# Optimization experiments

Hardware: AMD Instinct MI355X
Metric: run time of the kernel (lower is better)

## Reference

```python
import jax, jax.numpy as jnp
import numpy as np

B, S, D, H = 8, 1024, 1024, 16
DH = D // H  # 64
SCALE = (DH // H) ** (-0.5)  # faithful to torch: (key.size(-1) // num_heads) ** -0.5 = 4**-0.5 = 0.5
LN_EPS = 1e-5


def setup_inputs() -> dict:
    key = jax.random.key(0)
    ks = jax.random.split(key, 12)
    f = jnp.float32
    return {
        "key":   jax.random.normal(ks[0], (B, S, D), f),
        "value": jax.random.normal(ks[1], (B, S, D), f),
        "query": jax.random.normal(ks[2], (B, S, D), f),
        "Wq": jax.random.normal(ks[3], (D, D), f) * 0.02,
        "bq": jnp.zeros((D,), f),
        "Wk": jax.random.normal(ks[4], (D, D), f) * 0.02,
        "bk": jnp.zeros((D,), f),
        "Wv": jax.random.normal(ks[5], (D, D), f) * 0.02,
        "bv": jnp.zeros((D,), f),
        "Wo": jax.random.normal(ks[6], (D, D), f) * 0.02,
        "bo": jnp.zeros((D,), f),
        "ln_gamma": jnp.ones((D,), f),
        "ln_beta": jnp.zeros((D,), f),
    }


def _layer_norm(x, gamma, beta):
    mu = jnp.mean(x, axis=-1, keepdims=True)
    var = jnp.mean(jnp.square(x - mu), axis=-1, keepdims=True)
    return (x - mu) * jax.lax.rsqrt(var + LN_EPS) * gamma + beta


def reference(key, value, query, Wq, bq, Wk, bk, Wv, bv, Wo, bo, ln_gamma, ln_beta):
    residual = query
    # QKV projections (torch Linear: x @ W.T + b)
    k = key @ Wk.T + bk
    v = value @ Wv.T + bv
    q = query @ Wq.T + bq
    # Faithful raw view [B,S,H*dh] -> [B*H, S, dh] (row-major reshape, as in torch .view)
    k = k.reshape(B * H, S, DH)
    v = v.reshape(B * H, S, DH)
    q = q.reshape(B * H, S, DH)
    # scores: [B*H, S, S], softmax over last axis (dim=2)
    attn = jnp.einsum("bid,bjd->bij", q, k) * SCALE
    attn = jax.nn.softmax(attn, axis=2)
    context = jnp.einsum("bij,bjd->bid", attn, v)
    context = context.reshape(B, S, D)  # faithful raw view back
    out = context @ Wo.T + bo
    out = _layer_norm(residual + out, ln_gamma, ln_beta)
    return out, attn
```

## Files before the change

### kernel.cpp

```cpp
#include <hip/hip_runtime.h>
#include <stdint.h>

typedef unsigned short ushort_t;
typedef __attribute__((ext_vector_type(8))) short s16x8;
typedef __attribute__((ext_vector_type(8))) unsigned short u16x8;
typedef __attribute__((ext_vector_type(4))) unsigned short u16x4;
typedef __attribute__((ext_vector_type(4))) float f32x4;

#define AS1C(p) ((const __attribute__((address_space(1))) void*)(p))
#define AS3(p)  ((__attribute__((address_space(3))) void*)(p))

#define QSCALE 0.7213475204444817f

#define EXP2F(x) __builtin_amdgcn_exp2f(x)
#define LOG2F(x) __builtin_amdgcn_logf(x)

#define WAVE_LDS_FENCE()                                    \
  do {                                                      \
    asm volatile("s_waitcnt lgkmcnt(0)" ::: "memory");      \
    __builtin_amdgcn_sched_barrier(0);                      \
  } while (0)

#define SBAR()                                              \
  do {                                                      \
    __builtin_amdgcn_sched_barrier(0);                      \
    __builtin_amdgcn_s_barrier();                           \
    __builtin_amdgcn_sched_barrier(0);                      \
  } while (0)

__device__ __forceinline__ ushort_t f2bf(float f) {
  uint32_t u = __float_as_uint(f);
  u += 0x7fffu + ((u >> 16) & 1u);
  return (ushort_t)(u >> 16);
}
__device__ __forceinline__ float bf2f(ushort_t h) {
  return __uint_as_float(((uint32_t)h) << 16);
}

__global__ __launch_bounds__(256) void cvt3_kernel(const float* __restrict__ s0,
                                                   const float* __restrict__ s1,
                                                   const float* __restrict__ s2,
                                                   ushort_t* __restrict__ dst) {
  const int y = blockIdx.y;
  const float* src = y == 0 ? s0 : (y == 1 ? s1 : s2);
  const int i = blockIdx.x * 256 + threadIdx.x;
  const float4 v = ((const float4*)src)[i];
  ushort4 o;
  o.x = f2bf(v.x); o.y = f2bf(v.y); o.z = f2bf(v.z); o.w = f2bf(v.w);
  ((ushort4*)(dst + (size_t)y * 8388608))[i] = o;
}

__global__ __launch_bounds__(256) void cvtw_kernel(const float* __restrict__ w0,
                                                   const float* __restrict__ w1,
                                                   const float* __restrict__ w2,
                                                   const float* __restrict__ w3,
                                                   ushort_t* __restrict__ dqkv,
                                                   ushort_t* __restrict__ dwo) {
  const int y = blockIdx.y;
  const float* src = y == 0 ? w0 : (y == 1 ? w1 : (y == 2 ? w2 : w3));
  ushort_t* dst = y < 3 ? dqkv + (size_t)y * 1048576 : dwo;
  const float sc = y == 0 ? QSCALE : 1.0f;
  const int i = blockIdx.x * 256 + threadIdx.x;
  const float4 v = ((const float4*)src)[i];
  ushort4 o;
  o.x = f2bf(v.x * sc); o.y = f2bf(v.y * sc); o.z = f2bf(v.z * sc); o.w = f2bf(v.w * sc);
  ((ushort4*)dst)[i] = o;
}

__global__ __launch_bounds__(256) void biascat_kernel(const float* __restrict__ bq,
                                                      const float* __restrict__ bk,
                                                      const float* __restrict__ bv,
                                                      float* __restrict__ dst) {
  const int i = blockIdx.x * 256 + threadIdx.x;
  dst[i] = i < 1024 ? bq[i] * QSCALE : (i < 2048 ? bk[i - 1024] : bv[i - 2048]);
}

template <int OUT_BF16>
__global__ __launch_bounds__(512) void gemm_nt(const ushort_t* __restrict__ A0,
                                               const ushort_t* __restrict__ A1,
                                               const ushort_t* __restrict__ A2,
                                               const ushort_t* __restrict__ B,
                                               const float* __restrict__ bias,
                                               void* __restrict__ C0,
                                               void* __restrict__ C1,
                                               void* __restrict__ C2) {
  __shared__ ushort_t As[3][128 * 32];
  __shared__ ushort_t Bs[3][128 * 32];
  const int tid = threadIdx.x;
  const int w = tid >> 6, lane = tid & 63, g = lane >> 4, c = lane & 15;
  const int wm = w >> 1, wn = w & 1;
  const int m0 = blockIdx.y * 128, n0 = blockIdx.x * 128;
  const int sel = n0 >> 10, nloc0 = n0 & 1023;
  const ushort_t* A = sel == 0 ? A0 : (sel == 1 ? A1 : A2);
  char* C = (char*)(sel == 0 ? C0 : (sel == 1 ? C1 : C2));
  f32x4 acc[2][4] = {};

  const int srow = tid >> 2, scol = (tid & 3) << 3;
  const int sdst = (w * 64) * 8;

#define G_STAGE(buf, k0_)                                                                  \
  do {                                                                                     \
    __builtin_amdgcn_global_load_lds(AS1C(&A[(size_t)(m0 + srow) * 1024 + (k0_) + scol]),  \
                                     AS3(&As[buf][sdst]), 16, 0, 0);                       \
    __builtin_amdgcn_global_load_lds(AS1C(&B[(size_t)(n0 + srow) * 1024 + (k0_) + scol]),  \
                                     AS3(&Bs[buf][sdst]), 16, 0, 0);                       \
  } while (0)

  G_STAGE(0, 0);
  G_STAGE(1, 32);
  asm volatile("s_waitcnt vmcnt(2)" ::: "memory");
  SBAR();
  int cur = 0;
  for (int it = 0; it < 32; ++it) {
    if (it < 30) {
      const int sb = cur >= 1 ? cur - 1 : 2;
      G_STAGE(sb, 32 * (it + 2));
    }
    s16x8 af[2], bfr[4];
#pragma unroll
    for (int mi = 0; mi < 2; ++mi)
      af[mi] = *(const s16x8*)&As[cur][(wm * 32 + mi * 16 + c) * 32 + g * 8];
#pragma unroll
    for (int ni = 0; ni < 4; ++ni)
      bfr[ni] = *(const s16x8*)&Bs[cur][(wn * 64 + ni * 16 + c) * 32 + g * 8];
    __builtin_amdgcn_s_setprio(1);
#pragma unroll
    for (int mi = 0; mi < 2; ++mi)
#pragma unroll
      for (int ni = 0; ni < 4; ++ni)
        acc[mi][ni] = __builtin_amdgcn_mfma_f32_16x16x32_bf16(af[mi], bfr[ni], acc[mi][ni], 0, 0, 0);
    __builtin_amdgcn_s_setprio(0);
    if (it < 31) {
      if (it < 30)
        asm volatile("s_waitcnt vmcnt(2) lgkmcnt(0)" ::: "memory");
      else
        asm volatile("s_waitcnt vmcnt(0) lgkmcnt(0)" ::: "memory");
      SBAR();
    }
    cur = cur < 2 ? cur + 1 : 0;
  }
#undef G_STAGE

#pragma unroll
  for (int ni = 0; ni < 4; ++ni) {
    const int nn = wn * 64 + ni * 16 + c;
    const float bv = bias[n0 + nn];
#pragma unroll
    for (int mi = 0; mi < 2; ++mi) {
#pragma unroll
      for (int rr = 0; rr < 4; ++rr) {
        const int m = m0 + wm * 32 + mi * 16 + g * 4 + rr;
        const float val = acc[mi][ni][rr] + bv;
        if (OUT_BF16)
          ((ushort_t*)C)[(size_t)m * 1024 + nloc0 + nn] = f2bf(val);
        else
          ((float*)C)[(size_t)m * 1024 + nloc0 + nn] = val;
      }
    }
  }
}

__global__ __launch_bounds__(256) void transpose_v(const ushort_t* __restrict__ v,
                                                   ushort_t* __restrict__ vt) {
  __shared__ ushort_t T[64][72];
  const int n = blockIdx.y, ib = blockIdx.x;
  const int t = threadIdx.x;
  {
    const int row = t >> 2, cb = (t & 3) << 4;
    const ushort_t* src = v + (size_t)n * 65536 + (size_t)(ib * 64 + row) * 64 + cb;
    *(u16x8*)&T[row][cb] = *(const u16x8*)src;
    *(u16x8*)&T[row][cb + 8] = *(const u16x8*)(src + 8);
  }
  __syncthreads();
  {
    const int dh = t >> 2, ibs = (t & 3) << 4;
    u16x8 a, b;
#pragma unroll
    for (int e = 0; e < 8; ++e) { a[e] = T[ibs + e][dh]; b[e] = T[ibs + 8 + e][dh]; }
    ushort_t* dst = vt + (size_t)n * 65536 + (size_t)dh * 1024 + ib * 64 + ibs;
    *(u16x8*)dst = a;
    *(u16x8*)(dst + 8) = b;
  }
}

__global__ __launch_bounds__(256) void stats_kernel(const ushort_t* __restrict__ q,
                                                    const ushort_t* __restrict__ k,
                                                    float* __restrict__ bias_out) {
  __shared__ ushort_t Kb[3][64 * 64];
  const int wg = blockIdx.x;
  const int idx = ((wg & 7) << 6) | (wg >> 3);
  const int n = idx >> 2, qb = idx & 3;
  const int tid = threadIdx.x, w = tid >> 6, lane = tid & 63, g = lane >> 4, c = lane & 15;
  const int q0 = qb * 256 + w * 64;
  const ushort_t* qh = q + (size_t)n * 65536;
  const char* khb = (const char*)(k + (size_t)n * 65536);

  const int r0 = w * 16 + (lane >> 3);
  const int csw = (((lane & 7) ^ (lane >> 3)) << 4);

#define STAGE_KS(buf, jt_)                                                                  \
  do {                                                                                      \
    __builtin_amdgcn_global_load_lds(AS1C(khb + ((size_t)(jt_)*64 + r0) * 128 + csw),       \
                                     AS3(&Kb[buf][(w * 2 + 0) * 512]), 16, 0, 0);           \
    __builtin_amdgcn_global_load_lds(AS1C(khb + ((size_t)(jt_)*64 + r0 + 8) * 128 + csw),   \
                                     AS3(&Kb[buf][(w * 2 + 1) * 512]), 16, 0, 0);           \
  } while (0)
#define KFRAGS(buf, jn, h)                                                    \
  (*(const s16x8*)((const char*)&Kb[buf][0] +                                 \
                   (((((jn)*16 + c) * 128 + (h)*64 + g * 16)) ^ ((c & 7) << 4))))

  s16x8 aq[4][2];
#pragma unroll
  for (int fr = 0; fr < 4; ++fr) {
    aq[fr][0] = *(const s16x8*)&qh[(q0 + fr * 16 + c) * 64 + g * 8];
    aq[fr][1] = *(const s16x8*)&qh[(q0 + fr * 16 + c) * 64 + 32 + g * 8];
  }

  float l_acc[4][4] = {};

  STAGE_KS(0, 0);
  STAGE_KS(1, 1);
  asm volatile("s_waitcnt vmcnt(2)" ::: "memory");
  SBAR();
  int cur = 0;
  for (int jt = 0; jt < 16; ++jt) {
    if (jt < 14) {
      const int sb = cur >= 1 ? cur - 1 : 2;
      STAGE_KS(sb, jt + 2);
    }
#pragma unroll
    for (int fr = 0; fr < 4; ++fr) {
      f32x4 sfr[4];
      __builtin_amdgcn_s_setprio(1);
#pragma unroll
      for (int jn = 0; jn < 4; ++jn) {
        f32x4 z = {0.f, 0.f, 0.f, 0.f};
        z = __builtin_amdgcn_mfma_f32_16x16x32_bf16(aq[fr][0], KFRAGS(cur, jn, 0), z, 0, 0, 0);
        z = __builtin_amdgcn_mfma_f32_16x16x32_bf16(aq[fr][1], KFRAGS(cur, jn, 1), z, 0, 0, 0);
        sfr[jn] = z;
      }
      __builtin_amdgcn_s_setprio(0);
#pragma unroll
      for (int rr = 0; rr < 4; ++rr)
        l_acc[fr][rr] += EXP2F(sfr[0][rr]) + EXP2F(sfr[1][rr]) +
                         EXP2F(sfr[2][rr]) + EXP2F(sfr[3][rr]);
    }
    if (jt < 15) {
      if (jt < 14)
        asm volatile("s_waitcnt vmcnt(2) lgkmcnt(0)" ::: "memory");
      else
        asm volatile("s_waitcnt vmcnt(0) lgkmcnt(0)" ::: "memory");
      SBAR();
    }
    cur = cur < 2 ? cur + 1 : 0;
  }

#pragma unroll
  for (int fr = 0; fr < 4; ++fr)
#pragma unroll
    for (int rr = 0; rr < 4; ++rr) {
      float l = l_acc[fr][rr];
      l += __shfl_xor(l, 1);
      l += __shfl_xor(l, 2);
      l += __shfl_xor(l, 4);
      l += __shfl_xor(l, 8);
      if (c == 0)
        bias_out[(size_t)n * 1024 + q0 + fr * 16 + g * 4 + rr] = LOG2F(l);
    }
#undef STAGE_KS
#undef KFRAGS
}

__global__ __launch_bounds__(256) void attn_kernel(const ushort_t* __restrict__ q,
                                                   const ushort_t* __restrict__ k,
                                                   const ushort_t* __restrict__ vt,
                                                   const float* __restrict__ stats,
                                                   float* __restrict__ attn,
                                                   ushort_t* __restrict__ ctx) {
  __shared__ ushort_t Kb[2][64 * 64];
  __shared__ ushort_t Vb[2][64 * 64];
  __shared__ ushort_t Pb[4][16 * 64];
  const int wg = blockIdx.x;
  const int idx = ((wg & 7) << 7) | (wg >> 3);
  const int n = idx >> 3, qb = idx & 7;
  const int tid = threadIdx.x, w = tid >> 6, lane = tid & 63, g = lane >> 4, c = lane & 15;
  const int i0 = qb * 128 + w * 32;
  const ushort_t* qh = q + (size_t)n * 65536;
  const char* khb = (const char*)(k + (size_t)n * 65536);
  const char* vhb = (const char*)(vt + (size_t)n * 65536);
  char* pwb = (char*)&Pb[w][0];

  const int r0 = w * 16 + (lane >> 3);
  const int csw = (((lane & 7) ^ (lane >> 3)) << 4);

#define STAGE_K(buf, jt_)                                                                   \
  do {                                                                                      \
    __builtin_amdgcn_global_load_lds(AS1C(khb + ((size_t)(jt_)*64 + r0) * 128 + csw),       \
                                     AS3(&Kb[buf][(w * 2 + 0) * 512]), 16, 0, 0);           \
    __builtin_amdgcn_global_load_lds(AS1C(khb + ((size_t)(jt_)*64 + r0 + 8) * 128 + csw),   \
                                     AS3(&Kb[buf][(w * 2 + 1) * 512]), 16, 0, 0);           \
  } while (0)
#define STAGE_V(buf, jt_)                                                                   \
  do {                                                                                      \
    __builtin_amdgcn_global_load_lds(AS1C(vhb + (size_t)r0 * 2048 + (jt_)*128 + csw),       \
                                     AS3(&Vb[buf][(w * 2 + 0) * 512]), 16, 0, 0);           \
    __builtin_amdgcn_global_load_lds(AS1C(vhb + (size_t)(r0 + 8) * 2048 + (jt_)*128 + csw), \
                                     AS3(&Vb[buf][(w * 2 + 1) * 512]), 16, 0, 0);           \
  } while (0)
#define KFRAG(buf, jn, h)                                                     \
  (*(const s16x8*)((const char*)&Kb[buf][0] +                                 \
                   (((((jn)*16 + c) * 128 + (h)*64 + g * 16)) ^ ((c & 7) << 4))))
#define VFRAG(buf, dn, ks_)                                                   \
  (*(const s16x8*)((const char*)&Vb[buf][0] +                                 \
                   (((((dn)*16 + c) * 128 + (ks_)*64 + g * 16)) ^ ((c & 7) << 4))))

  s16x8 aq[2][2];
  float bias_r[2][4];
#pragma unroll
  for (int fr = 0; fr < 2; ++fr) {
    aq[fr][0] = *(const s16x8*)&qh[(i0 + fr * 16 + c) * 64 + g * 8];
    aq[fr][1] = *(const s16x8*)&qh[(i0 + fr * 16 + c) * 64 + 32 + g * 8];
    const float* sb = stats + (size_t)n * 1024 + i0 + fr * 16;
#pragma unroll
    for (int r = 0; r < 4; ++r) bias_r[fr][r] = sb[4 * g + r];
  }

  f32x4 cacc[2][4] = {};
  float* arow = attn + (size_t)n * 1048576;

  STAGE_K(0, 0);
  STAGE_V(0, 0);
  asm volatile("s_waitcnt vmcnt(0) lgkmcnt(0)" ::: "memory");
  SBAR();
  for (int jt = 0; jt < 16; ++jt) {
    const int cur = jt & 1;
    if (jt < 15) { STAGE_K(cur ^ 1, jt + 1); STAGE_V(cur ^ 1, jt + 1); }
    f32x4 s[2][4];
    __builtin_amdgcn_s_setprio(1);
#pragma unroll
    for (int fr = 0; fr < 2; ++fr)
#pragma unroll
      for (int jn = 0; jn < 4; ++jn) {
        f32x4 z = {0.f, 0.f, 0.f, 0.f};
        z = __builtin_amdgcn_mfma_f32_16x16x32_bf16(aq[fr][0], KFRAG(cur, jn, 0), z, 0, 0, 0);
        z = __builtin_amdgcn_mfma_f32_16x16x32_bf16(aq[fr][1], KFRAG(cur, jn, 1), z, 0, 0, 0);
        s[fr][jn] = z;
      }
    __builtin_amdgcn_s_setprio(0);
#pragma unroll
    for (int fr = 0; fr < 2; ++fr) {
#pragma unroll
      for (int jn = 0; jn < 4; ++jn)
#pragma unroll
        for (int r = 0; r < 4; ++r) {
          const float p = EXP2F(s[fr][jn][r] - bias_r[fr][r]);
          const int row = 4 * g + r;
          const int A = (row << 7) + ((jn * 16 + c) << 1);
          *(ushort_t*)(pwb + (A ^ ((row & 7) << 4))) = f2bf(p);
        }
      WAVE_LDS_FENCE();
      __builtin_amdgcn_s_setprio(1);
#pragma unroll
      for (int ks = 0; ks < 2; ++ks) {
        const int A = (c << 7) + (ks << 6) + (g << 4);
        const s16x8 pa = *(const s16x8*)(pwb + (A ^ ((c & 7) << 4)));
#pragma unroll
        for (int dn = 0; dn < 4; ++dn)
          cacc[fr][dn] =
              __builtin_amdgcn_mfma_f32_16x16x32_bf16(pa, VFRAG(cur, dn, ks), cacc[fr][dn], 0, 0, 0);
      }
      __builtin_amdgcn_s_setprio(0);
#pragma unroll
      for (int e = 0; e < 4; ++e) {
        const int row = g + 4 * e;
        const int A = (row << 7) + (c << 3);
        const u16x4 hv = *(const u16x4*)(pwb + (A ^ ((row & 7) << 4)));
        f32x4 fv;
#pragma unroll
        for (int t2 = 0; t2 < 4; ++t2) fv[t2] = bf2f(hv[t2]);
        __builtin_nontemporal_store(
            fv, (f32x4*)&arow[(size_t)(i0 + fr * 16 + row) * 1024 + jt * 64 + c * 4]);
      }
      WAVE_LDS_FENCE();
    }
    if (jt < 15) {
      asm volatile("s_waitcnt vmcnt(8) lgkmcnt(0)" ::: "memory");
      SBAR();
    }
  }

  ushort_t* ch = ctx + (size_t)n * 65536;
#pragma unroll
  for (int fr = 0; fr < 2; ++fr)
#pragma unroll
    for (int dn = 0; dn < 4; ++dn)
#pragma unroll
      for (int r = 0; r < 4; ++r)
        ch[(size_t)(i0 + fr * 16 + 4 * g + r) * 64 + dn * 16 + c] = f2bf(cacc[fr][dn][r]);
#undef STAGE_K
#undef STAGE_V
#undef KFRAG
#undef VFRAG
}

__global__ __launch_bounds__(256) void ln_kernel(const float* __restrict__ proj,
                                                 const float* __restrict__ resid,
                                                 const float* __restrict__ gamma,
                                                 const float* __restrict__ beta,
                                                 float* __restrict__ out) {
  __shared__ float sred[4], ssred[4];
  const int row = blockIdx.x, t = threadIdx.x;
  const float4 pv = ((const float4*)(proj + (size_t)row * 1024))[t];
  const float4 rv = ((const float4*)(resid + (size_t)row * 1024))[t];
  float4 x;
  x.x = pv.x + rv.x; x.y = pv.y + rv.y; x.z = pv.z + rv.z; x.w = pv.w + rv.w;
  float s = x.x + x.y + x.z + x.w;
  float ss = x.x * x.x + x.y * x.y + x.z * x.z + x.w * x.w;
#pragma unroll
  for (int msk = 1; msk < 64; msk <<= 1) {
    s += __shfl_xor(s, msk);
    ss += __shfl_xor(ss, msk);
  }
  const int w = t >> 6, lane = t & 63;
  if (lane == 0) { sred[w] = s; ssred[w] = ss; }
  __syncthreads();
  s = sred[0] + sred[1] + sred[2] + sred[3];
  ss = ssred[0] + ssred[1] + ssred[2] + ssred[3];
  const float mu = s * (1.f / 1024.f);
  const float var = ss * (1.f / 1024.f) - mu * mu;
  const float rs = rsqrtf(var + 1e-5f);
  const float4 gm = ((const float4*)gamma)[t];
  const float4 bt = ((const float4*)beta)[t];
  float4 o;
  o.x = (x.x - mu) * rs * gm.x + bt.x;
  o.y = (x.y - mu) * rs * gm.y + bt.y;
  o.z = (x.z - mu) * rs * gm.z + bt.z;
  o.w = (x.w - mu) * rs * gm.w + bt.w;
  ((float4*)(out + (size_t)row * 1024))[t] = o;
}

extern "C" void kernel_launch(void* const* d_in, const int* in_sizes, int n_in,
                              void* d_out, int out_size, void* d_ws, size_t ws_size,
                              hipStream_t stream) {
  const float* key   = (const float*)d_in[0];
  const float* value = (const float*)d_in[1];
  const float* query = (const float*)d_in[2];
  const float* Wq = (const float*)d_in[3];  const float* bq = (const float*)d_in[4];
  const float* Wk = (const float*)d_in[5];  const float* bk = (const float*)d_in[6];
  const float* Wv = (const float*)d_in[7];  const float* bv = (const float*)d_in[8];
  const float* Wo = (const float*)d_in[9];  const float* bo = (const float*)d_in[10];
  const float* gamma = (const float*)d_in[11];
  const float* beta  = (const float*)d_in[12];

  char* ws = (char*)d_ws;
  ushort_t* q_   = (ushort_t*)(ws + 0);
  ushort_t* k_   = (ushort_t*)(ws + 16777216);
  ushort_t* vt_  = (ushort_t*)(ws + 33554432);
  ushort_t* ctx_ = (ushort_t*)(ws + 50331648);
  ushort_t* wo_  = (ushort_t*)(ws + 67108864);
  float*    proj_ = (float*)(ws + 0);

  char* o8 = (char*)d_out;
  float*    outp  = (float*)o8;
  float*    attnp = (float*)(o8 + 33554432);
  float*    stats = (float*)o8;
  ushort_t* xq   = (ushort_t*)(o8 + 33554432);
  ushort_t* xk   = (ushort_t*)(o8 + 50331648);
  ushort_t* xv   = (ushort_t*)(o8 + 67108864);
  ushort_t* wqkv = (ushort_t*)(o8 + 83886080);
  ushort_t* v_   = (ushort_t*)(o8 + 90177536);
  float*    bqkv = (float*)(o8 + 106954752);

  cvt3_kernel<<<dim3(8192, 3), 256, 0, stream>>>(query, key, value, xq);
  cvtw_kernel<<<dim3(1024, 4), 256, 0, stream>>>(Wq, Wk, Wv, Wo, wqkv, wo_);
  biascat_kernel<<<12, 256, 0, stream>>>(bq, bk, bv, bqkv);

  gemm_nt<1><<<dim3(24, 64), 512, 0, stream>>>(xq, xk, xv, wqkv, bqkv, q_, k_, v_);

  transpose_v<<<dim3(16, 128), 256, 0, stream>>>(v_, vt_);

  stats_kernel<<<512, 256, 0, stream>>>(q_, k_, stats);

  attn_kernel<<<1024, 256, 0, stream>>>(q_, k_, vt_, stats, attnp, ctx_);

  gemm_nt<0><<<dim3(8, 64), 512, 0, stream>>>(ctx_, ctx_, ctx_, wo_, bo, proj_, proj_, proj_);

  ln_kernel<<<8192, 256, 0, stream>>>(proj_, query, gamma, beta, outp);
}
```

Measured before the change: 319.3 us.

## Fuse residual add into output GEMM and batch P·V MFMAs per tile

The residual add moves from the layernorm kernel into the output-projection GEMM epilogue, so the layernorm reads one 32 MB tensor instead of two. In the attention kernel, the P buffer now holds both 16-row fragments, so each K/V tile needs a single LDS fence pair instead of one per fragment. The P·V MFMAs for the two fragments are interleaved, sharing each V fragment load. The cost is twice the LDS for P and an uncoalesced scalar residual read in the GEMM epilogue.

```diff
diff --git a/kernel.cpp b/kernel.cpp
--- a/kernel.cpp
+++ b/kernel.cpp
@@ -75,12 +75,13 @@
   dst[i] = i < 1024 ? bq[i] * QSCALE : (i < 2048 ? bk[i - 1024] : bv[i - 2048]);
 }
 
-template <int OUT_BF16>
+template <int OUT_BF16, int ADD_RESID>
 __global__ __launch_bounds__(512) void gemm_nt(const ushort_t* __restrict__ A0,
                                                const ushort_t* __restrict__ A1,
                                                const ushort_t* __restrict__ A2,
                                                const ushort_t* __restrict__ B,
                                                const float* __restrict__ bias,
+                                               const float* __restrict__ resid,
                                                void* __restrict__ C0,
                                                void* __restrict__ C1,
                                                void* __restrict__ C2) {
@@ -150,7 +151,8 @@
 #pragma unroll
       for (int rr = 0; rr < 4; ++rr) {
         const int m = m0 + wm * 32 + mi * 16 + g * 4 + rr;
-        const float val = acc[mi][ni][rr] + bv;
+        float val = acc[mi][ni][rr] + bv;
+        if (ADD_RESID) val += resid[(size_t)m * 1024 + nloc0 + nn];
         if (OUT_BF16)
           ((ushort_t*)C)[(size_t)m * 1024 + nloc0 + nn] = f2bf(val);
         else
@@ -279,7 +281,7 @@
                                                    ushort_t* __restrict__ ctx) {
   __shared__ ushort_t Kb[2][64 * 64];
   __shared__ ushort_t Vb[2][64 * 64];
-  __shared__ ushort_t Pb[4][16 * 64];
+  __shared__ ushort_t Pb[4][32 * 64];
   const int wg = blockIdx.x;
   const int idx = ((wg & 7) << 7) | (wg >> 3);
   const int n = idx >> 3, qb = idx & 7;
@@ -348,41 +350,47 @@
       }
     __builtin_amdgcn_s_setprio(0);
 #pragma unroll
-    for (int fr = 0; fr < 2; ++fr) {
+    for (int fr = 0; fr < 2; ++fr)
 #pragma unroll
       for (int jn = 0; jn < 4; ++jn)
 #pragma unroll
         for (int r = 0; r < 4; ++r) {
           const float p = EXP2F(s[fr][jn][r] - bias_r[fr][r]);
-          const int row = 4 * g + r;
+          const int row = fr * 16 + 4 * g + r;
           const int A = (row << 7) + ((jn * 16 + c) << 1);
           *(ushort_t*)(pwb + (A ^ ((row & 7) << 4))) = f2bf(p);
         }
-      WAVE_LDS_FENCE();
-      __builtin_amdgcn_s_setprio(1);
-#pragma unroll
-      for (int ks = 0; ks < 2; ++ks) {
-        const int A = (c << 7) + (ks << 6) + (g << 4);
-        const s16x8 pa = *(const s16x8*)(pwb + (A ^ ((c & 7) << 4)));
-#pragma unroll
-        for (int dn = 0; dn < 4; ++dn)
-          cacc[fr][dn] =
-              __builtin_amdgcn_mfma_f32_16x16x32_bf16(pa, VFRAG(cur, dn, ks), cacc[fr][dn], 0, 0, 0);
-      }
-      __builtin_amdgcn_s_setprio(0);
+    WAVE_LDS_FENCE();
+    __builtin_amdgcn_s_setprio(1);
+#pragma unroll
+    for (int ks = 0; ks < 2; ++ks) {
+      s16x8 pa[2];
+#pragma unroll
+      for (int fr = 0; fr < 2; ++fr) {
+        const int A = ((fr * 16 + c) << 7) + (ks << 6) + (g << 4);
+        pa[fr] = *(const s16x8*)(pwb + (A ^ ((c & 7) << 4)));
+      }
+#pragma unroll
+      for (int dn = 0; dn < 4; ++dn) {
+        const s16x8 bv = VFRAG(cur, dn, ks);
+        cacc[0][dn] = __builtin_amdgcn_mfma_f32_16x16x32_bf16(pa[0], bv, cacc[0][dn], 0, 0, 0);
+        cacc[1][dn] = __builtin_amdgcn_mfma_f32_16x16x32_bf16(pa[1], bv, cacc[1][dn], 0, 0, 0);
+      }
+    }
+    __builtin_amdgcn_s_setprio(0);
+#pragma unroll
+    for (int fr = 0; fr < 2; ++fr)
 #pragma unroll
       for (int e = 0; e < 4; ++e) {
-        const int row = g + 4 * e;
+        const int row = fr * 16 + g + 4 * e;
         const int A = (row << 7) + (c << 3);
         const u16x4 hv = *(const u16x4*)(pwb + (A ^ ((row & 7) << 4)));
         f32x4 fv;
 #pragma unroll
         for (int t2 = 0; t2 < 4; ++t2) fv[t2] = bf2f(hv[t2]);
         __builtin_nontemporal_store(
-            fv, (f32x4*)&arow[(size_t)(i0 + fr * 16 + row) * 1024 + jt * 64 + c * 4]);
-      }
-      WAVE_LDS_FENCE();
-    }
+            fv, (f32x4*)&arow[(size_t)(i0 + row) * 1024 + jt * 64 + c * 4]);
+      }
     if (jt < 15) {
       asm volatile("s_waitcnt vmcnt(8) lgkmcnt(0)" ::: "memory");
       SBAR();
@@ -403,17 +411,13 @@
 #undef VFRAG
 }
 
-__global__ __launch_bounds__(256) void ln_kernel(const float* __restrict__ proj,
-                                                 const float* __restrict__ resid,
+__global__ __launch_bounds__(256) void ln_kernel(const float* __restrict__ xin,
                                                  const float* __restrict__ gamma,
                                                  const float* __restrict__ beta,
                                                  float* __restrict__ out) {
   __shared__ float sred[4], ssred[4];
   const int row = blockIdx.x, t = threadIdx.x;
-  const float4 pv = ((const float4*)(proj + (size_t)row * 1024))[t];
-  const float4 rv = ((const float4*)(resid + (size_t)row * 1024))[t];
-  float4 x;
-  x.x = pv.x + rv.x; x.y = pv.y + rv.y; x.z = pv.z + rv.z; x.w = pv.w + rv.w;
+  const float4 x = ((const float4*)(xin + (size_t)row * 1024))[t];
   float s = x.x + x.y + x.z + x.w;
   float ss = x.x * x.x + x.y * x.y + x.z * x.z + x.w * x.w;
 #pragma unroll
@@ -458,7 +462,7 @@
   ushort_t* vt_  = (ushort_t*)(ws + 33554432);
   ushort_t* ctx_ = (ushort_t*)(ws + 50331648);
   ushort_t* wo_  = (ushort_t*)(ws + 67108864);
-  float*    proj_ = (float*)(ws + 0);
+  float*    x_   = (float*)(ws + 0);
 
   char* o8 = (char*)d_out;
   float*    outp  = (float*)o8;
@@ -475,7 +479,8 @@
   cvtw_kernel<<<dim3(1024, 4), 256, 0, stream>>>(Wq, Wk, Wv, Wo, wqkv, wo_);
   biascat_kernel<<<12, 256, 0, stream>>>(bq, bk, bv, bqkv);
 
-  gemm_nt<1><<<dim3(24, 64), 512, 0, stream>>>(xq, xk, xv, wqkv, bqkv, q_, k_, v_);
+  gemm_nt<1, 0><<<dim3(24, 64), 512, 0, stream>>>(xq, xk, xv, wqkv, bqkv, nullptr,
+                                                  q_, k_, v_);
 
   transpose_v<<<dim3(16, 128), 256, 0, stream>>>(v_, vt_);
 
@@ -483,7 +488,8 @@
 
   attn_kernel<<<1024, 256, 0, stream>>>(q_, k_, vt_, stats, attnp, ctx_);
 
-  gemm_nt<0><<<dim3(8, 64), 512, 0, stream>>>(ctx_, ctx_, ctx_, wo_, bo, proj_, proj_, proj_);
-
-  ln_kernel<<<8192, 256, 0, stream>>>(proj_, query, gamma, beta, outp);
-}
+  gemm_nt<0, 1><<<dim3(8, 64), 512, 0, stream>>>(ctx_, ctx_, ctx_, wo_, bo, query,
+                                                 x_, x_, x_);
+
+  ln_kernel<<<8192, 256, 0, stream>>>(x_, gamma, beta, outp);
+}
```

Result: no change. 320.2 us (+0.3%).
